# Kernel optimization log

Hardware: AMD Instinct MI355X
Metric: run time of the kernel (lower is better)

The kernel has to match this reference:

```python
import jax, jax.numpy as jnp
import numpy as np

DIM = 384
HEADS = 6
HEAD_DIM = 64
WIN = 14
SCALE = HEAD_DIM ** -0.5
EPS = 1e-5  # torch LayerNorm default


def setup_inputs() -> dict:
    key = jax.random.key(0)
    ks = jax.random.split(key, 8)
    w = lambda k, shape: jax.random.normal(k, shape, dtype=jnp.float32) * 0.02
    return {
        "x": jax.random.normal(ks[0], (1, 336, 336, DIM), dtype=jnp.float32),
        "qkv_w": w(ks[1], (DIM, 3 * DIM)),
        "qkv_b": jnp.zeros((3 * DIM,), jnp.float32),
        "proj_w": w(ks[2], (DIM, DIM)),
        "proj_b": jnp.zeros((DIM,), jnp.float32),
        "rel_pos_h": w(ks[3], (2 * WIN - 1, HEAD_DIM)),
        "rel_pos_w": w(ks[4], (2 * WIN - 1, HEAD_DIM)),
        "norm1_w": jnp.ones((DIM,), jnp.float32),
        "norm1_b": jnp.zeros((DIM,), jnp.float32),
        "norm2_w": jnp.ones((DIM,), jnp.float32),
        "norm2_b": jnp.zeros((DIM,), jnp.float32),
        "fc1_w": w(ks[5], (DIM, 4 * DIM)),
        "fc1_b": jnp.zeros((4 * DIM,), jnp.float32),
        "fc2_w": w(ks[6], (4 * DIM, DIM)),
        "fc2_b": jnp.zeros((DIM,), jnp.float32),
    }


def _layernorm(x, w, b):
    m = jnp.mean(x, axis=-1, keepdims=True)
    v = jnp.var(x, axis=-1, keepdims=True)
    return (x - m) / jnp.sqrt(v + EPS) * w + b


def _rel_table(rel_pos):
    coords = np.arange(WIN)[:, None] - np.arange(WIN)[None, :] + (WIN - 1)
    return rel_pos[coords]


def _block(x, qkv_w, qkv_b, proj_w, proj_b, rel_pos_h, rel_pos_w,
           norm1_w, norm1_b, norm2_w, norm2_b, fc1_w, fc1_b, fc2_w, fc2_b):
    B, H, W, C = x.shape
    shortcut = x
    x = _layernorm(x, norm1_w, norm1_b)

    nH, nW = H // WIN, W // WIN
    xw = x.reshape(B, nH, WIN, nW, WIN, C).transpose(0, 1, 3, 2, 4, 5)
    xw = xw.reshape(B * nH * nW, WIN * WIN, C)  # [Nw, 196, C]
    Nw, L = xw.shape[0], WIN * WIN

    # --- attention with decomposed rel-pos ---
    qkv = xw @ qkv_w + qkv_b                         # [Nw, 196, 3C]
    qkv = qkv.reshape(Nw, L, 3, HEADS, HEAD_DIM).transpose(2, 0, 3, 1, 4)
    q, k, v = qkv[0], qkv[1], qkv[2]                 # [Nw, h, 196, d]

    attn = jnp.einsum("bhqd,bhkd->bhqk", q * SCALE, k)  # [Nw, h, 196, 196]

    Rh = _rel_table(rel_pos_h)                       # [14, 14, d]
    Rw = _rel_table(rel_pos_w)
    r_q = q.reshape(Nw, HEADS, WIN, WIN, HEAD_DIM)
    rel_h = jnp.einsum("bnhwc,hkc->bnhwk", r_q, Rh)  # [Nw, h, 14, 14, 14]
    rel_w = jnp.einsum("bnhwc,wkc->bnhwk", r_q, Rw)
    attn = (attn.reshape(Nw, HEADS, WIN, WIN, WIN, WIN)
            + rel_h[..., :, None] + rel_w[..., None, :]).reshape(Nw, HEADS, L, L)

    attn = jax.nn.softmax(attn, axis=-1)
    out = jnp.einsum("bhqk,bhkd->bhqd", attn, v)     # [Nw, h, 196, d]
    out = out.transpose(0, 2, 1, 3).reshape(Nw, L, C)
    out = out @ proj_w + proj_b

    # --- window unpartition ---
    out = out.reshape(B, nH, nW, WIN, WIN, C).transpose(0, 1, 3, 2, 4, 5)
    out = out.reshape(B, H, W, C)

    x = shortcut + out
    h = _layernorm(x, norm2_w, norm2_b)
    h = jax.nn.gelu(h @ fc1_w + fc1_b, approximate=False) @ fc2_w + fc2_b
    return x + h


def reference(x, qkv_w, qkv_b, proj_w, proj_b, rel_pos_h, rel_pos_w,
              norm1_w, norm1_b, norm2_w, norm2_b, fc1_w, fc1_b, fc2_w, fc2_b):
    return _block(x, qkv_w, qkv_b, proj_w, proj_b, rel_pos_h, rel_pos_w,
                  norm1_w, norm1_b, norm2_w, norm2_b, fc1_w, fc1_b, fc2_w, fc2_b)
```

## Files before the change

kernel.cpp:

```cpp
#include <hip/hip_runtime.h>
#include <math.h>

#define TOKENS 112896
#define C      384
#define NQKV   1152
#define NFC    1536
#define HEADS  6
#define HD     64
#define WIN    14
#define L      196
#define NWS    24
#define SCALEF 0.125f

typedef unsigned int  u32;
typedef unsigned short u16;
typedef short short8 __attribute__((ext_vector_type(8)));
typedef float floatx4 __attribute__((ext_vector_type(4)));

__device__ __forceinline__ u16 f2bf(float f) {
  u32 u = __float_as_uint(f);
  u += 0x7FFFu + ((u >> 16) & 1u);
  return (u16)(u >> 16);
}

__device__ __forceinline__ float bf2f(u16 v) {
  return __uint_as_float((u32)v << 16);
}

__device__ __forceinline__ void async16(u16* lds, const u16* g) {
  __builtin_amdgcn_global_load_lds((const __attribute__((address_space(1))) void*)g,
                                   (__attribute__((address_space(3))) void*)lds,
                                   16, 0, 0);
}

__device__ __forceinline__ int win_to_tok(int r) {
  int n = r / L, l = r % L;
  int wh = n / NWS, ww = n % NWS;
  int ih = l / WIN, iw = l % WIN;
  return (wh * WIN + ih) * 336 + ww * WIN + iw;
}

__global__ __launch_bounds__(256) void conv_t_kernel(const float* __restrict__ in,
    u16* __restrict__ out, int K, int N)
{
  int idx = blockIdx.x * 256 + threadIdx.x;
  if (idx >= K * N) return;
  int n = idx / K, k = idx % K;
  out[idx] = f2bf(in[(size_t)k * N + n]);
}

template<bool PERMUTE>
__global__ __launch_bounds__(128) void ln_kernel(const float* __restrict__ x,
    const float* __restrict__ w, const float* __restrict__ b,
    u16* __restrict__ out)
{
  const int t = blockIdx.x;
  const int tid = threadIdx.x;
  const float* xr = x + (size_t)t * C;
  float v0 = xr[tid], v1 = xr[tid + 128], v2 = xr[tid + 256];
  float s  = v0 + v1 + v2;
  float ss = v0 * v0 + v1 * v1 + v2 * v2;
#pragma unroll
  for (int off = 32; off > 0; off >>= 1) {
    s  += __shfl_down(s, off);
    ss += __shfl_down(ss, off);
  }
  __shared__ float red[4];
  if ((tid & 63) == 0) { red[(tid >> 6) * 2 + 0] = s; red[(tid >> 6) * 2 + 1] = ss; }
  __syncthreads();
  float S  = red[0] + red[2];
  float SS = red[1] + red[3];
  float mean = S * (1.0f / C);
  float var  = SS * (1.0f / C) - mean * mean;
  float rstd = rsqrtf(var + 1e-5f);
  size_t orow;
  if (PERMUTE) {
    int h_ = t / 336, w_ = t % 336;
    int wh = h_ / WIN, ih = h_ % WIN;
    int ww = w_ / WIN, iw = w_ % WIN;
    orow = (size_t)((wh * NWS + ww) * L + ih * WIN + iw);
  } else {
    orow = (size_t)t;
  }
  u16* op = out + orow * C;
  op[tid]       = f2bf((v0 - mean) * rstd * w[tid]       + b[tid]);
  op[tid + 128] = f2bf((v1 - mean) * rstd * w[tid + 128] + b[tid + 128]);
  op[tid + 256] = f2bf((v2 - mean) * rstd * w[tid + 256] + b[tid + 256]);
}

template<int MODE>
__global__ __launch_bounds__(256) void gemm_bf16(
    const u16* __restrict__ A, const u16* __restrict__ Bt,
    const float* __restrict__ bias, const float* __restrict__ res,
    void* __restrict__ outv, int N, int K)
{
  __shared__ u16 As[128 * 32];
  __shared__ u16 Bs[128 * 32];
  const int tid = threadIdx.x;
  const int w = tid >> 6, l = tid & 63;
  const int bm = blockIdx.y * 128, bn = blockIdx.x * 128;
  const int wm = (w >> 1) * 64, wn = (w & 1) * 64;
  const int lm = l & 15, quad = l >> 4;

  floatx4 acc[4][4] = {};

  const int srow = tid >> 2, sseg = tid & 3;
  const u16* Ag0 = A  + (size_t)(bm + srow)      * K + sseg * 8;
  const u16* Ag1 = A  + (size_t)(bm + srow + 64) * K + sseg * 8;
  const u16* Bg0 = Bt + (size_t)(bn + srow)      * K + sseg * 8;
  const u16* Bg1 = Bt + (size_t)(bn + srow + 64) * K + sseg * 8;
  u16* Asw0 = As + w * 512;
  u16* Asw1 = As + 2048 + w * 512;
  u16* Bsw0 = Bs + w * 512;
  u16* Bsw1 = Bs + 2048 + w * 512;

  for (int kt = 0; kt < K; kt += 32) {
    async16(Asw0, Ag0 + kt);
    async16(Asw1, Ag1 + kt);
    async16(Bsw0, Bg0 + kt);
    async16(Bsw1, Bg1 + kt);
    __syncthreads();
    short8 af[4], bf[4];
#pragma unroll
    for (int i = 0; i < 4; i++)
      af[i] = *(const short8*)(As + (wm + i * 16 + lm) * 32 + quad * 8);
#pragma unroll
    for (int j = 0; j < 4; j++)
      bf[j] = *(const short8*)(Bs + (wn + j * 16 + lm) * 32 + quad * 8);
#pragma unroll
    for (int i = 0; i < 4; i++)
#pragma unroll
      for (int j = 0; j < 4; j++)
        acc[i][j] = __builtin_amdgcn_mfma_f32_16x16x32_bf16(af[i], bf[j], acc[i][j], 0, 0, 0);
    __syncthreads();
  }

  const int colbase = bn + wn + lm;
  float bb[4];
#pragma unroll
  for (int j = 0; j < 4; j++) bb[j] = bias[colbase + j * 16];

#pragma unroll
  for (int i = 0; i < 4; i++) {
#pragma unroll
    for (int reg = 0; reg < 4; reg++) {
      int row = bm + wm + i * 16 + quad * 4 + reg;
      size_t ro;
      if (MODE == 1) ro = (size_t)win_to_tok(row) * N;
      else           ro = (size_t)row * N;
#pragma unroll
      for (int j = 0; j < 4; j++) {
        float v = acc[i][j][reg] + bb[j];
        int col = colbase + j * 16;
        if (MODE == 0) {
          ((u16*)outv)[ro + col] = f2bf(v);
        } else if (MODE == 1) {
          ((float*)outv)[ro + col] = v + res[ro + col];
        } else if (MODE == 2) {
          ((u16*)outv)[ro + col] = f2bf(0.5f * v * (1.0f + erff(v * 0.70710678118654752f)));
        } else {
          ((float*)outv)[ro + col] = v + res[ro + col];
        }
      }
    }
  }
}

__global__ __launch_bounds__(256, 2) void attn_kernel(
    const u16* __restrict__ qkv,
    const float* __restrict__ relh, const float* __restrict__ relw,
    u16* __restrict__ out)
{
  __shared__ float Plds[4][512];
  __shared__ u16 rhlds[208 * 28];
  __shared__ u16 rwlds[208 * 28];
  __shared__ u16 Klds[32 * 64];
  __shared__ u16 Vtl[64 * 40];

  const int n = blockIdx.x / HEADS;
  const int h = blockIdx.x % HEADS;
  const int tid = threadIdx.x;
  const int w = tid >> 6;
  const int l = tid & 63;
  const int lm = l & 15;
  const int quad = l >> 4;
  const size_t base = (size_t)n * L;

  short8 qf[4][2];
#pragma unroll
  for (int i = 0; i < 4; i++) {
    int rt = w + 4 * i;
    if (rt <= 12) {
      int row = rt * 16 + lm; if (row > 195) row = 195;
      const u16* qp = qkv + (base + row) * NQKV + h * HD + quad * 8;
#pragma unroll
      for (int kf = 0; kf < 2; kf++)
        qf[i][kf] = *(const short8*)(qp + kf * 32);
    }
  }

  {
    short8 tf[2][2][2];
#pragma unroll
    for (int tab = 0; tab < 2; tab++) {
      const float* tp = tab ? relw : relh;
#pragma unroll
      for (int ct = 0; ct < 2; ct++) {
        int t = ct * 16 + lm;
#pragma unroll
        for (int kf = 0; kf < 2; kf++) {
          short8 v = {0, 0, 0, 0, 0, 0, 0, 0};
          if (t < 27) {
            const float* p = tp + t * HD + kf * 32 + quad * 8;
            float4 a = *(const float4*)p;
            float4 b = *(const float4*)(p + 4);
            v[0] = (short)f2bf(a.x); v[1] = (short)f2bf(a.y);
            v[2] = (short)f2bf(a.z); v[3] = (short)f2bf(a.w);
            v[4] = (short)f2bf(b.x); v[5] = (short)f2bf(b.y);
            v[6] = (short)f2bf(b.z); v[7] = (short)f2bf(b.w);
          }
          tf[tab][ct][kf] = v;
        }
      }
    }
#pragma unroll
    for (int i = 0; i < 4; i++) {
      int rt = w + 4 * i;
      if (rt > 12) continue;
#pragma unroll
      for (int tab = 0; tab < 2; tab++) {
        u16* dst = tab ? rwlds : rhlds;
#pragma unroll
        for (int ct = 0; ct < 2; ct++) {
          floatx4 acc = {};
          acc = __builtin_amdgcn_mfma_f32_16x16x32_bf16(qf[i][0], tf[tab][ct][0], acc, 0, 0, 0);
          acc = __builtin_amdgcn_mfma_f32_16x16x32_bf16(qf[i][1], tf[tab][ct][1], acc, 0, 0, 0);
          int t = ct * 16 + lm;
          if (t < 28) {
#pragma unroll
            for (int reg = 0; reg < 4; reg++) {
              int q = rt * 16 + quad * 4 + reg;
              dst[q * 28 + t] = f2bf(acc[reg]);
            }
          }
        }
      }
    }
  }

  floatx4 oacc[4][4] = {};
  float lsum[4][4] = {};

#pragma unroll 1
  for (int ks = 0; ks < 7; ks++) {
    __syncthreads();
    {
      int r = tid >> 3, g = tid & 7;
      int row = ks * 32 + r; if (row > 195) row = 195;
      uint4 kd = *(const uint4*)(qkv + (base + row) * NQKV + C + h * HD + g * 8);
      *(uint4*)&Klds[r * 64 + ((g ^ (r & 7)) * 8)] = kd;
    }
    {
      int r = tid & 31, seg = tid >> 5;
      int row = ks * 32 + r; if (row > 195) row = 195;
      uint4 vd = *(const uint4*)(qkv + (base + row) * NQKV + 2 * C + h * HD + seg * 8);
      union { uint4 u; u16 s[8]; } vv; vv.u = vd;
#pragma unroll
      for (int j = 0; j < 8; j++) Vtl[(seg * 8 + j) * 40 + r] = vv.s[j];
    }
    __syncthreads();

    short8 kfr[2][2];
#pragma unroll
    for (int ct = 0; ct < 2; ct++) {
      int krow = ct * 16 + lm;
#pragma unroll
      for (int kf = 0; kf < 2; kf++)
        kfr[ct][kf] = *(const short8*)&Klds[krow * 64 + (((kf * 4 + quad) ^ (krow & 7)) * 8)];
    }
    short8 vfr[4];
#pragma unroll
    for (int dt = 0; dt < 4; dt++)
      vfr[dt] = *(const short8*)&Vtl[(dt * 16 + lm) * 40 + quad * 8];

#pragma unroll
    for (int i = 0; i < 4; i++) {
      int rt = w + 4 * i;
      if (rt > 12) continue;
      floatx4 sc[2] = {};
#pragma unroll
      for (int ct = 0; ct < 2; ct++) {
        sc[ct] = __builtin_amdgcn_mfma_f32_16x16x32_bf16(qf[i][0], kfr[ct][0], sc[ct], 0, 0, 0);
        sc[ct] = __builtin_amdgcn_mfma_f32_16x16x32_bf16(qf[i][1], kfr[ct][1], sc[ct], 0, 0, 0);
      }
      float* Pw = Plds[w];
#pragma unroll
      for (int ct = 0; ct < 2; ct++) {
        int k = ks * 32 + ct * 16 + lm;
        int kh = (k * 293) >> 12;
        int kw2 = k - kh * 14;
        bool kval = (k < 196);
#pragma unroll
        for (int reg = 0; reg < 4; reg++) {
          int q = rt * 16 + quad * 4 + reg;
          int qh = (q * 293) >> 12;
          int qw = q - qh * 14;
          int th = qh - kh + 13; th = th < 0 ? 0 : th;
          int tw = qw - kw2 + 13;
          float bh = bf2f(rhlds[q * 28 + th]);
          float bw = bf2f(rwlds[q * 28 + tw]);
          float s = sc[ct][reg] * SCALEF + bh + bw;
          float p = kval ? __expf(s) : 0.0f;
          lsum[i][reg] += p;
          int prow = quad * 4 + reg;
          int col = ct * 16 + lm;
          Pw[prow * 32 + (((col >> 2) ^ (prow & 7)) * 4) + (col & 3)] = p;
        }
      }
      floatx4 pa = *(const floatx4*)&Pw[lm * 32 + (((2 * quad) ^ (lm & 7)) * 4)];
      floatx4 pb = *(const floatx4*)&Pw[lm * 32 + (((2 * quad + 1) ^ (lm & 7)) * 4)];
      short8 pfr;
#pragma unroll
      for (int j = 0; j < 4; j++) {
        pfr[j]     = (short)f2bf(pa[j]);
        pfr[4 + j] = (short)f2bf(pb[j]);
      }
#pragma unroll
      for (int dt = 0; dt < 4; dt++)
        oacc[i][dt] = __builtin_amdgcn_mfma_f32_16x16x32_bf16(pfr, vfr[dt], oacc[i][dt], 0, 0, 0);
    }
  }

#pragma unroll
  for (int i = 0; i < 4; i++) {
    int rt = w + 4 * i;
    if (rt > 12) continue;
#pragma unroll
    for (int reg = 0; reg < 4; reg++) {
      float v = lsum[i][reg];
      v += __shfl_xor(v, 1);
      v += __shfl_xor(v, 2);
      v += __shfl_xor(v, 4);
      v += __shfl_xor(v, 8);
      float inv = 1.0f / v;
      int row = rt * 16 + quad * 4 + reg;
      if (row < 196) {
        u16* op = out + (base + row) * C + h * HD + lm;
#pragma unroll
        for (int dt = 0; dt < 4; dt++) op[dt * 16] = f2bf(oacc[i][dt][reg] * inv);
      }
    }
  }
}

extern "C" void kernel_launch(void* const* d_in, const int* in_sizes, int n_in,
                              void* d_out, int out_size, void* d_ws, size_t ws_size,
                              hipStream_t stream)
{
  const float* x      = (const float*)d_in[0];
  const float* qkv_w  = (const float*)d_in[1];
  const float* qkv_b  = (const float*)d_in[2];
  const float* proj_w = (const float*)d_in[3];
  const float* proj_b = (const float*)d_in[4];
  const float* rel_h  = (const float*)d_in[5];
  const float* rel_w  = (const float*)d_in[6];
  const float* n1w    = (const float*)d_in[7];
  const float* n1b    = (const float*)d_in[8];
  const float* n2w    = (const float*)d_in[9];
  const float* n2b    = (const float*)d_in[10];
  const float* fc1_w  = (const float*)d_in[11];
  const float* fc1_b  = (const float*)d_in[12];
  const float* fc2_w  = (const float*)d_in[13];
  const float* fc2_b  = (const float*)d_in[14];

  u16*  W0 = (u16*)d_ws;
  u16*  W1 = (u16*)((char*)d_ws + 86704128);
  float* W2 = (float*)((char*)d_ws + 86704128 + 346816512);
  u16*  WT = (u16*)((char*)d_ws + 86704128 + 346816512 + 173408256);
  u16* qkv_wT  = WT;
  u16* proj_wT = qkv_wT + 442368;
  u16* fc1_wT  = proj_wT + 147456;
  u16* fc2_wT  = fc1_wT + 589824;

  conv_t_kernel<<<(442368 + 255) / 256, 256, 0, stream>>>(qkv_w, qkv_wT, C, NQKV);
  conv_t_kernel<<<(147456 + 255) / 256, 256, 0, stream>>>(proj_w, proj_wT, C, C);
  conv_t_kernel<<<(589824 + 255) / 256, 256, 0, stream>>>(fc1_w, fc1_wT, C, NFC);
  conv_t_kernel<<<(589824 + 255) / 256, 256, 0, stream>>>(fc2_w, fc2_wT, NFC, C);

  ln_kernel<true><<<TOKENS, 128, 0, stream>>>(x, n1w, n1b, W0);
  gemm_bf16<0><<<dim3(NQKV / 128, TOKENS / 128), 256, 0, stream>>>(
      W0, qkv_wT, qkv_b, nullptr, W1, NQKV, C);
  attn_kernel<<<576 * HEADS, 256, 0, stream>>>(W1, rel_h, rel_w, W0);
  gemm_bf16<1><<<dim3(C / 128, TOKENS / 128), 256, 0, stream>>>(
      W0, proj_wT, proj_b, x, W2, C, C);
  ln_kernel<false><<<TOKENS, 128, 0, stream>>>(W2, n2w, n2b, W0);
  gemm_bf16<2><<<dim3(NFC / 128, TOKENS / 128), 256, 0, stream>>>(
      W0, fc1_wT, fc1_b, nullptr, W1, NFC, C);
  gemm_bf16<3><<<dim3(C / 128, TOKENS / 128), 256, 0, stream>>>(
      W1, fc2_wT, fc2_b, W2, (float*)d_out, C, NFC);
}
```

Before: 1.505 ms.

## Double-buffer GEMM with BK=64, swizzled LDS, XCD-aware block remap, tiled transpose

Reworks the bf16 GEMM main loop to stage K-tiles of 64 into double-buffered LDS with asynchronous global-to-LDS loads, so the next tile loads while MFMAs run on the current one. It also XOR-swizzles the LDS layout to avoid bank conflicts, remaps workgroup IDs so neighbouring tiles land on the same XCD for L2 reuse, and sets launch bounds to 2 blocks per CU. The weight transpose kernel now goes through a shared-memory tile so both reads and writes are coalesced. LDS per block grows to 64KB, which may limit occupancy. The loop now issues the next stage's async loads right after the previous barrier, with only one barrier per iteration, so correctness depends on those loads being ordered properly against the reads of the buffer being computed.

```diff
diff --git a/kernel.cpp b/kernel.cpp
--- a/kernel.cpp
+++ b/kernel.cpp
@@ -43,10 +43,20 @@
 __global__ __launch_bounds__(256) void conv_t_kernel(const float* __restrict__ in,
     u16* __restrict__ out, int K, int N)
 {
-  int idx = blockIdx.x * 256 + threadIdx.x;
-  if (idx >= K * N) return;
-  int n = idx / K, k = idx % K;
-  out[idx] = f2bf(in[(size_t)k * N + n]);
+  __shared__ u16 tile[32][33];
+  const int kb = blockIdx.y * 32, nb = blockIdx.x * 32;
+  const int tx = threadIdx.x & 31, ty = threadIdx.x >> 5;
+#pragma unroll
+  for (int i = 0; i < 4; i++) {
+    int k = kb + ty + i * 8;
+    tile[ty + i * 8][tx] = f2bf(in[(size_t)k * N + nb + tx]);
+  }
+  __syncthreads();
+#pragma unroll
+  for (int i = 0; i < 4; i++) {
+    int n = nb + ty + i * 8;
+    out[(size_t)n * K + kb + tx] = tile[tx][ty + i * 8];
+  }
 }
 
 template<bool PERMUTE>
@@ -89,49 +99,77 @@
 }
 
 template<int MODE>
-__global__ __launch_bounds__(256) void gemm_bf16(
+__global__ __launch_bounds__(256, 2) void gemm_bf16(
     const u16* __restrict__ A, const u16* __restrict__ Bt,
     const float* __restrict__ bias, const float* __restrict__ res,
     void* __restrict__ outv, int N, int K)
 {
-  __shared__ u16 As[128 * 32];
-  __shared__ u16 Bs[128 * 32];
+  __shared__ u16 As[2][128 * 64];
+  __shared__ u16 Bs[2][128 * 64];
   const int tid = threadIdx.x;
   const int w = tid >> 6, l = tid & 63;
-  const int bm = blockIdx.y * 128, bn = blockIdx.x * 128;
+
+  const int nwg = gridDim.x * gridDim.y;
+  int lin = blockIdx.y * gridDim.x + blockIdx.x;
+  {
+    int q8 = nwg >> 3, r8 = nwg & 7;
+    int xcd = lin & 7, sub = lin >> 3;
+    lin = (xcd < r8 ? xcd * (q8 + 1) : r8 * (q8 + 1) + (xcd - r8) * q8) + sub;
+  }
+  const int bx = lin % gridDim.x, by = lin / gridDim.x;
+  const int bm = by * 128, bn = bx * 128;
+
   const int wm = (w >> 1) * 64, wn = (w & 1) * 64;
   const int lm = l & 15, quad = l >> 4;
 
   floatx4 acc[4][4] = {};
 
-  const int srow = tid >> 2, sseg = tid & 3;
-  const u16* Ag0 = A  + (size_t)(bm + srow)      * K + sseg * 8;
-  const u16* Ag1 = A  + (size_t)(bm + srow + 64) * K + sseg * 8;
-  const u16* Bg0 = Bt + (size_t)(bn + srow)      * K + sseg * 8;
-  const u16* Bg1 = Bt + (size_t)(bn + srow + 64) * K + sseg * 8;
-  u16* Asw0 = As + w * 512;
-  u16* Asw1 = As + 2048 + w * 512;
-  u16* Bsw0 = Bs + w * 512;
-  u16* Bsw1 = Bs + 2048 + w * 512;
-
-  for (int kt = 0; kt < K; kt += 32) {
-    async16(Asw0, Ag0 + kt);
-    async16(Asw1, Ag1 + kt);
-    async16(Bsw0, Bg0 + kt);
-    async16(Bsw1, Bg1 + kt);
-    __syncthreads();
-    short8 af[4], bf[4];
+  const int srow8 = l >> 3;
+  const int sgran = (l & 7) ^ srow8;
+  const u16* Ag[4];
+  const u16* Bg[4];
+#pragma unroll
+  for (int p = 0; p < 4; p++) {
+    Ag[p] = A  + (size_t)(bm + p * 32 + w * 8 + srow8) * K + sgran * 8;
+    Bg[p] = Bt + (size_t)(bn + p * 32 + w * 8 + srow8) * K + sgran * 8;
+  }
+
+  auto stage = [&](int buf, int kt) {
+#pragma unroll
+    for (int p = 0; p < 4; p++) {
+      async16(&As[buf][(p * 32 + w * 8) * 64], Ag[p] + kt);
+      async16(&Bs[buf][(p * 32 + w * 8) * 64], Bg[p] + kt);
+    }
+  };
+
+  const int nk = K >> 6;
+  stage(0, 0);
+  __syncthreads();
+
+  for (int t = 0; t < nk; t++) {
+    const int buf = t & 1;
+    if (t + 1 < nk) stage(buf ^ 1, (t + 1) << 6);
+
+    short8 af[4][2], bf[4][2];
+#pragma unroll
+    for (int i = 0; i < 4; i++) {
+      int r = wm + i * 16 + lm, sw = r & 7;
+      af[i][0] = *(const short8*)(&As[buf][r * 64 + ((quad ^ sw) * 8)]);
+      af[i][1] = *(const short8*)(&As[buf][r * 64 + (((4 + quad) ^ sw) * 8)]);
+    }
+#pragma unroll
+    for (int j = 0; j < 4; j++) {
+      int r = wn + j * 16 + lm, sw = r & 7;
+      bf[j][0] = *(const short8*)(&Bs[buf][r * 64 + ((quad ^ sw) * 8)]);
+      bf[j][1] = *(const short8*)(&Bs[buf][r * 64 + (((4 + quad) ^ sw) * 8)]);
+    }
 #pragma unroll
     for (int i = 0; i < 4; i++)
-      af[i] = *(const short8*)(As + (wm + i * 16 + lm) * 32 + quad * 8);
-#pragma unroll
-    for (int j = 0; j < 4; j++)
-      bf[j] = *(const short8*)(Bs + (wn + j * 16 + lm) * 32 + quad * 8);
-#pragma unroll
-    for (int i = 0; i < 4; i++)
-#pragma unroll
-      for (int j = 0; j < 4; j++)
-        acc[i][j] = __builtin_amdgcn_mfma_f32_16x16x32_bf16(af[i], bf[j], acc[i][j], 0, 0, 0);
+#pragma unroll
+      for (int j = 0; j < 4; j++) {
+        acc[i][j] = __builtin_amdgcn_mfma_f32_16x16x32_bf16(af[i][0], bf[j][0], acc[i][j], 0, 0, 0);
+        acc[i][j] = __builtin_amdgcn_mfma_f32_16x16x32_bf16(af[i][1], bf[j][1], acc[i][j], 0, 0, 0);
+      }
     __syncthreads();
   }
 
@@ -382,10 +420,10 @@
   u16* fc1_wT  = proj_wT + 147456;
   u16* fc2_wT  = fc1_wT + 589824;
 
-  conv_t_kernel<<<(442368 + 255) / 256, 256, 0, stream>>>(qkv_w, qkv_wT, C, NQKV);
-  conv_t_kernel<<<(147456 + 255) / 256, 256, 0, stream>>>(proj_w, proj_wT, C, C);
-  conv_t_kernel<<<(589824 + 255) / 256, 256, 0, stream>>>(fc1_w, fc1_wT, C, NFC);
-  conv_t_kernel<<<(589824 + 255) / 256, 256, 0, stream>>>(fc2_w, fc2_wT, NFC, C);
+  conv_t_kernel<<<dim3(NQKV / 32, C / 32), 256, 0, stream>>>(qkv_w, qkv_wT, C, NQKV);
+  conv_t_kernel<<<dim3(C / 32, C / 32), 256, 0, stream>>>(proj_w, proj_wT, C, C);
+  conv_t_kernel<<<dim3(NFC / 32, C / 32), 256, 0, stream>>>(fc1_w, fc1_wT, C, NFC);
+  conv_t_kernel<<<dim3(C / 32, NFC / 32), 256, 0, stream>>>(fc2_w, fc2_wT, NFC, C);
 
   ln_kernel<true><<<TOKENS, 128, 0, stream>>>(x, n1w, n1b, W0);
   gemm_bf16<0><<<dim3(NQKV / 128, TOKENS / 128), 256, 0, stream>>>(
```

Result: no change. 1.482 ms (-1.5%).
